# Optimization experiments

Hardware: AMD Instinct MI355X
Metric: run time of the kernel (lower is better)

The kernel has to match this reference:

```python
import jax, jax.numpy as jnp
import numpy as np

N, C, T, V = 16, 128, 128, 25
K, H, OC = 3, 8, 256          # kernel_size subsets, heads, out_channels
HOPMAX = 12                   # hop values in [0, 12); emb_table size HOPMAX
EPS_BN = 1e-5
EPS_NORM = 1e-4


def setup_inputs() -> dict:
    key = jax.random.key(0)
    ks = jax.random.split(key, 12)
    s = 0.05
    x = jax.random.normal(ks[0], (N, C, T, V), jnp.float32)
    hop = jax.random.randint(ks[1], (V, V), 0, HOPMAX)
    emb_table = jax.random.normal(ks[2], (K, H, HOPMAX), jnp.float32) * s
    # A initialized as identity (as in the module) plus small noise for nontrivial grads
    A = jnp.tile(jnp.eye(V, dtype=jnp.float32), (K, H, 1, 1)) \
        + jax.random.normal(ks[3], (K, H, V, V), jnp.float32) * s
    w_block = jax.random.normal(ks[4], (K * OC, C // H), jnp.float32) * s  # grouped 1x1 conv, groups=K*H
    b_block = jax.random.normal(ks[5], (K * OC,), jnp.float32) * s
    bn_gamma = jnp.ones((OC,), jnp.float32)
    bn_beta = jnp.zeros((OC,), jnp.float32)
    res_w = jax.random.normal(ks[6], (OC, C), jnp.float32) * s  # residual 1x1 conv
    res_b = jax.random.normal(ks[7], (OC,), jnp.float32) * s
    res_bn_gamma = jnp.ones((OC,), jnp.float32)
    res_bn_beta = jnp.zeros((OC,), jnp.float32)
    return {"x": x, "hop": hop, "emb_table": emb_table, "A": A,
            "w_block": w_block, "b_block": b_block,
            "bn_gamma": bn_gamma, "bn_beta": bn_beta,
            "res_w": res_w, "res_b": res_b,
            "res_bn_gamma": res_bn_gamma, "res_bn_beta": res_bn_beta}


def _batchnorm(x, gamma, beta):
    # training-mode BatchNorm2d: batch stats over (N, T, V), biased variance
    m = jnp.mean(x, axis=(0, 2, 3), keepdims=True)
    v = jnp.var(x, axis=(0, 2, 3), keepdims=True)
    xn = (x - m) * jax.lax.rsqrt(v + EPS_BN)
    return gamma[None, :, None, None] * xn + beta[None, :, None, None]


def _l2_col_norm(w):
    # torch.norm(w, p=2, dim=-2, keepdim=True) + 1e-4  (in-degree normalization)
    return jnp.sqrt(jnp.sum(w * w, axis=-2, keepdims=True)) + EPS_NORM


def reference(x, hop, emb_table, A, w_block, b_block, bn_gamma, bn_beta,
              res_w, res_b, res_bn_gamma, res_bn_beta):
    n, c, t, v = x.shape
    # residual: 1x1 TemporalConv2d + BN (in_channels != out_channels)
    res = jnp.einsum('nctv,oc->notv', x, res_w) + res_b[None, :, None, None]
    res = _batchnorm(res, res_bn_gamma, res_bn_beta)

    # hop-embedding gather -> [K, H, V, V]; fuse normalized B and A
    B = emb_table[:, :, hop]
    BnA = B / _l2_col_norm(B) + A / _l2_col_norm(A)

    # graph conv: einsum over joint dim v (broadcast over k)
    xh = x.reshape(n, H, c // H, t, v)                      # [N,H,C/H,T,V]
    y = jnp.einsum('nhctv,khvw->nkhctw', xh, BnA)           # [N,K,H,C/H,T,V]
    y = y.reshape(n, K * H, c // H, t, v)                   # groups = K*H

    # grouped 1x1 conv: per-group [C/H -> OC/H] GEMM
    wg = w_block.reshape(K * H, OC // H, c // H)
    out = jnp.einsum('ngctv,goc->ngotv', y, wg)             # [N,K*H,OC/H,T,V]
    out = out.reshape(n, K * OC, t, v) + b_block[None, :, None, None]

    # sum over the K kernel subsets
    out = out.reshape(n, K, OC, t, v).sum(axis=1)
    out = _batchnorm(out, bn_gamma, bn_beta)
    return jax.nn.relu(out + res)
```

## Files before the change

kernel.cpp:

```cpp
#include <hip/hip_runtime.h>
#include <stdint.h>

typedef __attribute__((ext_vector_type(8))) short short8;
typedef __attribute__((ext_vector_type(4))) float f32x4;

#define B_BNA    0ull
#define B_STATS  60416ull
#define B_RESW2  64512ull
#define B_E2     1178624ull
#define B_XB     7994368ull
#define B_MAIN   21625856ull
#define B_RES    47840256ull

#define NTV 51200.0f

__device__ __forceinline__ unsigned short f2bf(float f) {
    unsigned u = __float_as_uint(f);
    return (unsigned short)((u + 0x7fffu + ((u >> 16) & 1u)) >> 16);
}
__device__ __forceinline__ float bf2f(unsigned s) { return __uint_as_float(s << 16); }

__device__ __forceinline__ float wave_sum(float v) {
#pragma unroll
    for (int m = 1; m < 64; m <<= 1) v += __shfl_xor(v, m, 64);
    return v;
}

__device__ __forceinline__ void gl_lds16(const unsigned short* g, unsigned short* l) {
    __builtin_amdgcn_global_load_lds(
        (const __attribute__((address_space(1))) unsigned int*)g,
        (__attribute__((address_space(3))) unsigned int*)l, 16, 0, 0);
}
__device__ __forceinline__ void stage_pair(const unsigned short* g0, const unsigned short* g1,
                                           unsigned short* d) {
    gl_lds16(g0, d);
    gl_lds16(g1, d + 512);
}

__device__ __forceinline__ int swz_idx(int row, int quad) {
    int rowX = row ^ ((row >> 2) & 1);
    return rowX * 32 + ((quad ^ (row & 3)) << 3);
}

__global__ __launch_bounds__(256) void k_prep(const int* __restrict__ hop,
                                              const float* __restrict__ emb,
                                              const float* __restrict__ A,
                                              const float* __restrict__ res_w,
                                              float* __restrict__ bna,
                                              float* __restrict__ stats,
                                              unsigned short* __restrict__ resw2) {
    int g = blockIdx.x, tid = threadIdx.x;
    if (g < 24) {
        if (tid < 25) {
            int w = tid;
            float nb = 0.f, na = 0.f;
            for (int v = 0; v < 25; v++) {
                float e = emb[g*12 + hop[v*25 + w]];
                nb += e*e;
                float a = A[((size_t)g*25 + v)*25 + w];
                na += a*a;
            }
            nb = sqrtf(nb) + 1e-4f;
            na = sqrtf(na) + 1e-4f;
            for (int v = 0; v < 25; v++) {
                float e = emb[g*12 + hop[v*25 + w]];
                float a = A[((size_t)g*25 + v)*25 + w];
                bna[g*625 + v*25 + w] = e/nb + a/na;
            }
        }
    } else if (g == 24) {
#pragma unroll
        for (int i = 0; i < 4; i++) stats[i*256 + tid] = 0.f;
    } else {
        int base = (g - 25) * 4096 + tid * 16;
#pragma unroll
        for (int j = 0; j < 16; j++) resw2[base + j] = f2bf(res_w[base + j]);
    }
}

__global__ __launch_bounds__(256) void k_prep2x(const float* __restrict__ w_block,
                                                const float* __restrict__ bna,
                                                unsigned short* __restrict__ E2,
                                                const float* __restrict__ x,
                                                unsigned short* __restrict__ xb) {
    int bid = blockIdx.x, tid = threadIdx.x;
    if (bid < 128) {
        __shared__ float bl[3*625];
        __shared__ float wl[3*64];
        int half = bid & 1, og = (bid >> 1) & 7, h = bid >> 4;

        for (int i = tid; i < 1875; i += 256) {
            int k3 = i / 625, j = i - k3*625;
            bl[i] = bna[(k3*8 + h)*625 + j];
        }
        if (tid < 192) {
            int k3 = tid >> 6, o = (tid >> 4) & 3, c = tid & 15;
            wl[tid] = w_block[(k3*256 + h*32 + og*4 + o)*16 + c];
        }
        __syncthreads();

        unsigned short* dst = E2 + (size_t)(h*8 + og)*53248;
        int e0 = half * 26624;
        for (int e = e0 + tid; e < e0 + 26624; e += 256) {
            int kc = e >> 12;
            int n  = (e >> 5) & 127;
            int kk = e & 31;
            int k  = kc*32 + kk;
            int o  = n >> 5, w = n & 31;
            float val = 0.f;
            if (k < 400 && w < 25) {
                int c = k / 25, v = k - c*25;
                val = wl[0*64 + o*16 + c] * bl[0*625 + v*25 + w]
                    + wl[1*64 + o*16 + c] * bl[1*625 + v*25 + w]
                    + wl[2*64 + o*16 + c] * bl[2*625 + v*25 + w];
            }
            dst[e] = f2bf(val);
        }
    } else {
        int b = bid - 128;
        int n_ = b >> 7, t_ = b & 127;
        unsigned short* row = xb + (size_t)b * 3328;
        for (int idx = tid; idx < 3200; idx += 256) {
            int c = idx / 25, v = idx - c*25;
            float val = x[(((size_t)n_*128 + c)*128 + t_)*25 + v];
            row[(c >> 4)*416 + (c & 15)*25 + v] = f2bf(val);
        }
        if (tid < 128) row[(tid >> 4)*416 + 400 + (tid & 15)] = 0;
    }
}

__global__ __launch_bounds__(256) void k_mm(const unsigned short* __restrict__ xb,
                                            const unsigned short* __restrict__ E2,
                                            unsigned short* __restrict__ mainp,
                                            const float* __restrict__ x,
                                            const unsigned short* __restrict__ resw2,
                                            unsigned short* __restrict__ resp,
                                            float* __restrict__ stats) {
    __shared__ unsigned short lds[24576];
    int bid = blockIdx.x, tid = threadIdx.x;
    int lane = tid & 63, wave = tid >> 6;
    int wm = wave >> 1, wn = wave & 1;
    int lane15 = lane & 15, quad = lane >> 4;

    int Lrow0 = wave*32 + (lane >> 2), Lq = lane & 3;
    int r0 = Lrow0 ^ ((Lrow0 >> 2) & 1), q0 = Lq ^ (r0 & 3);
    int Lrow1 = Lrow0 + 16;
    int r1 = Lrow1 ^ ((Lrow1 >> 2) & 1), q1 = Lq ^ (r1 & 3);

    const int adoff = wave*1024 + lane*8;

    if (bid < 1024) {
        int h = bid & 7, og = (bid >> 3) & 7, mt = bid >> 6;

        const unsigned short* agA0 = xb + (size_t)(mt*128 + r0)*3328 + h*416 + q0*8;
        const unsigned short* agA1 = xb + (size_t)(mt*128 + r1)*3328 + h*416 + q1*8;
        const unsigned short* eb   = E2 + (size_t)(h*8 + og)*53248;
        const unsigned short* bgB0 = eb + r0*32 + q0*8;
        const unsigned short* bgB1 = eb + r1*32 + q1*8;

        f32x4 acc[4][4] = {};

#pragma unroll
        for (int p = 0; p < 3; p++) {
            int bo = p*8192;
            stage_pair(agA0 + p*32,           agA1 + p*32,           lds + bo + adoff);
            stage_pair(bgB0 + (size_t)p*4096, bgB1 + (size_t)p*4096, lds + bo + 4096 + adoff);
        }

        int bufo = 0;
        for (int kc = 0; kc < 13; kc++) {
            if (kc <= 10)      asm volatile("s_waitcnt vmcnt(8)" ::: "memory");
            else if (kc == 11) asm volatile("s_waitcnt vmcnt(4)" ::: "memory");
            else               asm volatile("s_waitcnt vmcnt(0)" ::: "memory");
            __builtin_amdgcn_s_barrier();

            const unsigned short* Ac = lds + bufo;
            const unsigned short* Bc = lds + bufo + 4096;
            short8 af[4], bq[4];
#pragma unroll
            for (int i = 0; i < 4; i++) {
                af[i] = *(const short8*)&Ac[swz_idx(wm*64 + i*16 + lane15, quad)];
                bq[i] = *(const short8*)&Bc[swz_idx(wn*64 + i*16 + lane15, quad)];
            }
            asm volatile("s_waitcnt lgkmcnt(0)" ::: "memory");
            __builtin_amdgcn_sched_barrier(0);
            __builtin_amdgcn_s_barrier();

            if (kc <= 9) {
                stage_pair(agA0 + (kc+3)*32,            agA1 + (kc+3)*32,
                           lds + bufo + adoff);
                stage_pair(bgB0 + (size_t)(kc+3)*4096,  bgB1 + (size_t)(kc+3)*4096,
                           lds + bufo + 4096 + adoff);
            }
#pragma unroll
            for (int i = 0; i < 4; i++)
#pragma unroll
                for (int j = 0; j < 4; j++)
                    acc[i][j] = __builtin_amdgcn_mfma_f32_16x16x32_bf16(af[i], bq[j], acc[i][j], 0, 0, 0);

            bufo += 8192;
            if (bufo == 24576) bufo = 0;
        }

        float s1[2] = {0.f, 0.f}, s2[2] = {0.f, 0.f};
#pragma unroll
        for (int j = 0; j < 4; j++) {
            int w = (j & 1)*16 + lane15;
            int p = j >> 1;
            if (w < 25) {
                int oc = h*32 + og*4 + wn*2 + p;
#pragma unroll
                for (int i = 0; i < 4; i++) {
                    int tb = wm*64 + i*16 + quad*4;
#pragma unroll
                    for (int r = 0; r < 4; r++) {
                        float val = acc[i][j][r];
                        mainp[((size_t)(mt*256 + oc)*128 + tb + r)*25 + w] = f2bf(val);
                        s1[p] += val;
                        s2[p] = fmaf(val, val, s2[p]);
                    }
                }
            }
        }
#pragma unroll
        for (int p = 0; p < 2; p++) {
            float a = wave_sum(s1[p]);
            float b = wave_sum(s2[p]);
            if (lane == 0) {
                int oc = h*32 + og*4 + wn*2 + p;
                atomicAdd(&stats[oc], a);
                atomicAdd(&stats[256 + oc], b);
            }
        }
    } else {
        int b2 = bid - 1024;
        int nt = (b2 >= 400) ? 1 : 0;
        int mt = b2 - nt*400;

        int n  = mt / 25;
        int off = (mt - n*25) * 128;
        const float* xb2 = x + (size_t)n*409600 + off;

        int c2 = tid >> 4, seg = tid & 15;

        const unsigned short* rb0 = resw2 + (size_t)(nt*128 + r0)*128 + q0*8;
        const unsigned short* rb1 = resw2 + (size_t)(nt*128 + r1)*128 + q1*8;

        f32x4 acc[4][4] = {};

        for (int kc = 0; kc < 4; kc++) {
            stage_pair(rb0 + kc*32, rb1 + kc*32, lds + 4096 + adoff);
            const float* xc0 = xb2 + (size_t)(kc*32 + 2*c2)*3200;
            const float* xc1 = xc0 + 3200;
            int wbase = 2*(c2 & 3), qn = c2 >> 2;
#pragma unroll
            for (int j = 0; j < 8; j++) {
                int m = seg + 16*j;
                unsigned pk = (unsigned)f2bf(xc0[m]) | ((unsigned)f2bf(xc1[m]) << 16);
                *(unsigned*)&lds[swz_idx(m, qn) + wbase] = pk;
            }
            __syncthreads();

            short8 af[4], bq[4];
#pragma unroll
            for (int i = 0; i < 4; i++) {
                af[i] = *(const short8*)&lds[swz_idx(wm*64 + i*16 + lane15, quad)];
                bq[i] = *(const short8*)&lds[4096 + swz_idx(wn*64 + i*16 + lane15, quad)];
            }
#pragma unroll
            for (int i = 0; i < 4; i++)
#pragma unroll
                for (int j = 0; j < 4; j++)
                    acc[i][j] = __builtin_amdgcn_mfma_f32_16x16x32_bf16(af[i], bq[j], acc[i][j], 0, 0, 0);
            __syncthreads();
        }

#pragma unroll
        for (int j = 0; j < 4; j++) {
            int oc = nt*128 + wn*64 + j*16 + lane15;
            float s1 = 0.f, s2 = 0.f;
#pragma unroll
            for (int i = 0; i < 4; i++) {
                int m2b = mt*128 + wm*64 + i*16 + quad*4;
#pragma unroll
                for (int r = 0; r < 4; r++) {
                    float val = acc[i][j][r];
                    int m2e = m2b + r;
                    int b = m2e / 25, v = m2e - b*25;
                    int nn = b >> 7, t = b & 127;
                    resp[((size_t)(nn*256 + oc)*128 + t)*25 + v] = f2bf(val);
                    s1 += val;
                    s2 = fmaf(val, val, s2);
                }
            }
            s1 += __shfl_xor(s1, 16, 64); s1 += __shfl_xor(s1, 32, 64);
            s2 += __shfl_xor(s2, 16, 64); s2 += __shfl_xor(s2, 32, 64);
            if (quad == 0) {
                atomicAdd(&stats[512 + oc], s1);
                atomicAdd(&stats[768 + oc], s2);
            }
        }
    }
}

__global__ __launch_bounds__(256) void k_final(const float* __restrict__ bn_g,
                                               const float* __restrict__ bn_b,
                                               const float* __restrict__ rbn_g,
                                               const float* __restrict__ rbn_b,
                                               const float* __restrict__ stats,
                                               const unsigned short* __restrict__ mainp,
                                               const unsigned short* __restrict__ resp,
                                               float* __restrict__ out) {
    __shared__ float4 cf[8];
    int bid = blockIdx.x, tid = threadIdx.x;
    int base_row = (bid * 1024) / 400;
    if (tid < 8) {
        int row = base_row + tid;
        if (row < 4096) {
            int oc = row & 255;
            const float inv = 1.f / NTV;
            float s1 = stats[oc],       s2 = stats[256 + oc];
            float r1v = stats[512 + oc], r2v = stats[768 + oc];
            float mm = s1*inv, vm = s2*inv - mm*mm;
            float mr = r1v*inv, vr = r2v*inv - mr*mr;
            float a1 = bn_g[oc]  * rsqrtf(vm + 1e-5f);
            float c1 = bn_b[oc]  - a1*mm;
            float a2 = rbn_g[oc] * rsqrtf(vr + 1e-5f);
            float c2 = rbn_b[oc] - a2*mr;
            cf[tid] = make_float4(a1, c1, a2, c2);
        }
    }
    __syncthreads();

    const uint4* m4 = (const uint4*)mainp;
    const uint4* r4 = (const uint4*)resp;
    float4* o4 = (float4*)out;
#pragma unroll
    for (int r = 0; r < 4; r++) {
        int chunk = bid*1024 + r*256 + tid;
        uint4 mu = m4[chunk];
        uint4 ru = r4[chunk];
        float4 C = cf[chunk/400 - base_row];
        float4 f0, f1;
        f0.x = fmaxf(fmaf(C.x, __uint_as_float(mu.x << 16),        C.y)
                   + fmaf(C.z, __uint_as_float(ru.x << 16),        C.w), 0.f);
        f0.y = fmaxf(fmaf(C.x, __uint_as_float(mu.x & 0xffff0000u), C.y)
                   + fmaf(C.z, __uint_as_float(ru.x & 0xffff0000u), C.w), 0.f);
        f0.z = fmaxf(fmaf(C.x, __uint_as_float(mu.y << 16),        C.y)
                   + fmaf(C.z, __uint_as_float(ru.y << 16),        C.w), 0.f);
        f0.w = fmaxf(fmaf(C.x, __uint_as_float(mu.y & 0xffff0000u), C.y)
                   + fmaf(C.z, __uint_as_float(ru.y & 0xffff0000u), C.w), 0.f);
        f1.x = fmaxf(fmaf(C.x, __uint_as_float(mu.z << 16),        C.y)
                   + fmaf(C.z, __uint_as_float(ru.z << 16),        C.w), 0.f);
        f1.y = fmaxf(fmaf(C.x, __uint_as_float(mu.z & 0xffff0000u), C.y)
                   + fmaf(C.z, __uint_as_float(ru.z & 0xffff0000u), C.w), 0.f);
        f1.z = fmaxf(fmaf(C.x, __uint_as_float(mu.w << 16),        C.y)
                   + fmaf(C.z, __uint_as_float(ru.w << 16),        C.w), 0.f);
        f1.w = fmaxf(fmaf(C.x, __uint_as_float(mu.w & 0xffff0000u), C.y)
                   + fmaf(C.z, __uint_as_float(ru.w & 0xffff0000u), C.w), 0.f);
        o4[chunk*2]     = f0;
        o4[chunk*2 + 1] = f1;
    }
}

extern "C" void kernel_launch(void* const* d_in, const int* in_sizes, int n_in,
                              void* d_out, int out_size, void* d_ws, size_t ws_size,
                              hipStream_t stream) {
    const float* x        = (const float*)d_in[0];
    const int*   hop      = (const int*)  d_in[1];
    const float* emb      = (const float*)d_in[2];
    const float* A        = (const float*)d_in[3];
    const float* w_block  = (const float*)d_in[4];
    const float* bn_g     = (const float*)d_in[6];
    const float* bn_b     = (const float*)d_in[7];
    const float* res_w    = (const float*)d_in[8];
    const float* rbn_g    = (const float*)d_in[10];
    const float* rbn_b    = (const float*)d_in[11];
    float* out = (float*)d_out;

    char* ws = (char*)d_ws;
    float*          bna    = (float*)(ws + B_BNA);
    float*          stats  = (float*)(ws + B_STATS);
    unsigned short* resw2  = (unsigned short*)(ws + B_RESW2);
    unsigned short* E2     = (unsigned short*)(ws + B_E2);
    unsigned short* xb     = (unsigned short*)(ws + B_XB);
    unsigned short* mainp  = (unsigned short*)(ws + B_MAIN);
    unsigned short* resp   = (unsigned short*)(ws + B_RES);

    k_prep   <<<33,   256, 0, stream>>>(hop, emb, A, res_w, bna, stats, resw2);
    k_prep2x <<<2176, 256, 0, stream>>>(w_block, bna, E2, x, xb);
    k_mm     <<<1824, 256, 0, stream>>>(xb, E2, mainp, x, resw2, resp, stats);
    k_final  <<<1600, 256, 0, stream>>>(bn_g, bn_b, rbn_g, rbn_b, stats, mainp, resp, out);
}
```

Before: 206.3 us.

## Load MFMA operands directly from global into registers, dropping LDS staging

The main GEMM path no longer stages A and B tiles through a triple-buffered shared-memory ring with barriers. Each wave now loads its own fragments straight from global memory into registers, double-buffered in software, which removes the LDS round trip and the block barriers and shrinks LDS to just what the residual path needs, allowing more resident blocks. In exchange, waves sharing a tile each fetch the same data from global or L2, giving up the reuse LDS provided. Per-lane 16-byte loads strided by 3328 elements may also coalesce poorly, and load latency is hidden by only one step of prefetch.

```diff
diff --git a/kernel.cpp b/kernel.cpp
--- a/kernel.cpp
+++ b/kernel.cpp
@@ -136,70 +136,56 @@
                                             const unsigned short* __restrict__ resw2,
                                             unsigned short* __restrict__ resp,
                                             float* __restrict__ stats) {
-    __shared__ unsigned short lds[24576];
+    __shared__ unsigned short lds[8192];
     int bid = blockIdx.x, tid = threadIdx.x;
     int lane = tid & 63, wave = tid >> 6;
     int wm = wave >> 1, wn = wave & 1;
     int lane15 = lane & 15, quad = lane >> 4;
 
-    int Lrow0 = wave*32 + (lane >> 2), Lq = lane & 3;
-    int r0 = Lrow0 ^ ((Lrow0 >> 2) & 1), q0 = Lq ^ (r0 & 3);
-    int Lrow1 = Lrow0 + 16;
-    int r1 = Lrow1 ^ ((Lrow1 >> 2) & 1), q1 = Lq ^ (r1 & 3);
-
-    const int adoff = wave*1024 + lane*8;
-
     if (bid < 1024) {
         int h = bid & 7, og = (bid >> 3) & 7, mt = bid >> 6;
 
-        const unsigned short* agA0 = xb + (size_t)(mt*128 + r0)*3328 + h*416 + q0*8;
-        const unsigned short* agA1 = xb + (size_t)(mt*128 + r1)*3328 + h*416 + q1*8;
-        const unsigned short* eb   = E2 + (size_t)(h*8 + og)*53248;
-        const unsigned short* bgB0 = eb + r0*32 + q0*8;
-        const unsigned short* bgB1 = eb + r1*32 + q1*8;
+        const unsigned short* Abase = xb + (size_t)(mt*128 + wm*64 + lane15)*3328
+                                         + h*416 + quad*8;
+        const unsigned short* Bbase = E2 + (size_t)(h*8 + og)*53248
+                                         + (wn*64 + lane15)*32 + quad*8;
+
+        auto loadA = [&](short8* d, int kc) {
+#pragma unroll
+            for (int i = 0; i < 4; i++)
+                d[i] = *(const short8*)(Abase + (size_t)i*16*3328 + kc*32);
+        };
+        auto loadB = [&](short8* d, int kc) {
+#pragma unroll
+            for (int j = 0; j < 4; j++)
+                d[j] = *(const short8*)(Bbase + j*512 + (size_t)kc*4096);
+        };
 
         f32x4 acc[4][4] = {};
-
-#pragma unroll
-        for (int p = 0; p < 3; p++) {
-            int bo = p*8192;
-            stage_pair(agA0 + p*32,           agA1 + p*32,           lds + bo + adoff);
-            stage_pair(bgB0 + (size_t)p*4096, bgB1 + (size_t)p*4096, lds + bo + 4096 + adoff);
-        }
-
-        int bufo = 0;
-        for (int kc = 0; kc < 13; kc++) {
-            if (kc <= 10)      asm volatile("s_waitcnt vmcnt(8)" ::: "memory");
-            else if (kc == 11) asm volatile("s_waitcnt vmcnt(4)" ::: "memory");
-            else               asm volatile("s_waitcnt vmcnt(0)" ::: "memory");
-            __builtin_amdgcn_s_barrier();
-
-            const unsigned short* Ac = lds + bufo;
-            const unsigned short* Bc = lds + bufo + 4096;
-            short8 af[4], bq[4];
-#pragma unroll
-            for (int i = 0; i < 4; i++) {
-                af[i] = *(const short8*)&Ac[swz_idx(wm*64 + i*16 + lane15, quad)];
-                bq[i] = *(const short8*)&Bc[swz_idx(wn*64 + i*16 + lane15, quad)];
-            }
-            asm volatile("s_waitcnt lgkmcnt(0)" ::: "memory");
-            __builtin_amdgcn_sched_barrier(0);
-            __builtin_amdgcn_s_barrier();
-
-            if (kc <= 9) {
-                stage_pair(agA0 + (kc+3)*32,            agA1 + (kc+3)*32,
-                           lds + bufo + adoff);
-                stage_pair(bgB0 + (size_t)(kc+3)*4096,  bgB1 + (size_t)(kc+3)*4096,
-                           lds + bufo + 4096 + adoff);
+        short8 aA[4], bA[4], aB[4], bB[4];
+
+        loadA(aA, 0); loadB(bA, 0);
+        for (int kc = 0; kc < 13; kc += 2) {
+            if (kc + 1 < 13) {
+                loadA(aB, kc + 1); loadB(bB, kc + 1);
+                __builtin_amdgcn_sched_barrier(0);
             }
 #pragma unroll
             for (int i = 0; i < 4; i++)
 #pragma unroll
                 for (int j = 0; j < 4; j++)
-                    acc[i][j] = __builtin_amdgcn_mfma_f32_16x16x32_bf16(af[i], bq[j], acc[i][j], 0, 0, 0);
-
-            bufo += 8192;
-            if (bufo == 24576) bufo = 0;
+                    acc[i][j] = __builtin_amdgcn_mfma_f32_16x16x32_bf16(aA[i], bA[j], acc[i][j], 0, 0, 0);
+            if (kc + 1 < 13) {
+                if (kc + 2 < 13) {
+                    loadA(aA, kc + 2); loadB(bA, kc + 2);
+                    __builtin_amdgcn_sched_barrier(0);
+                }
+#pragma unroll
+                for (int i = 0; i < 4; i++)
+#pragma unroll
+                    for (int j = 0; j < 4; j++)
+                        acc[i][j] = __builtin_amdgcn_mfma_f32_16x16x32_bf16(aB[i], bB[j], acc[i][j], 0, 0, 0);
+            }
         }
 
         float s1[2] = {0.f, 0.f}, s2[2] = {0.f, 0.f};
@@ -236,6 +222,12 @@
         int b2 = bid - 1024;
         int nt = (b2 >= 400) ? 1 : 0;
         int mt = b2 - nt*400;
+
+        int Lrow0 = wave*32 + (lane >> 2), Lq = lane & 3;
+        int r0 = Lrow0 ^ ((Lrow0 >> 2) & 1), q0 = Lq ^ (r0 & 3);
+        int Lrow1 = Lrow0 + 16;
+        int r1 = Lrow1 ^ ((Lrow1 >> 2) & 1), q1 = Lq ^ (r1 & 3);
+        const int adoff = wave*1024 + lane*8;
 
         int n  = mt / 25;
         int off = (mt - n*25) * 128;
```

Result: slower. 247.7 us (+20.0%).

## Fuse prep kernels and switch GEMM staging to double buffering

Applied to the files above, without the earlier changes.

Merges the BnA/stats/res-weight prep kernel into the E2/xb prep kernel, so each E2 block recomputes its head's normalized adjacency directly into shared memory. This removes one launch and a global intermediate buffer. The main GEMM kernel moves from a triple- to a double-buffered LDS pipeline, reducing LDS use to allow higher occupancy at the cost of a shallower prefetch depth.

```diff
diff --git a/kernel.cpp b/kernel.cpp
--- a/kernel.cpp
+++ b/kernel.cpp
@@ -4,7 +4,6 @@
 typedef __attribute__((ext_vector_type(8))) short short8;
 typedef __attribute__((ext_vector_type(4))) float f32x4;
 
-#define B_BNA    0ull
 #define B_STATS  60416ull
 #define B_RESW2  64512ull
 #define B_E2     1178624ull
@@ -42,17 +41,25 @@
     return rowX * 32 + ((quad ^ (row & 3)) << 3);
 }
 
-__global__ __launch_bounds__(256) void k_prep(const int* __restrict__ hop,
-                                              const float* __restrict__ emb,
-                                              const float* __restrict__ A,
-                                              const float* __restrict__ res_w,
-                                              float* __restrict__ bna,
-                                              float* __restrict__ stats,
-                                              unsigned short* __restrict__ resw2) {
-    int g = blockIdx.x, tid = threadIdx.x;
-    if (g < 24) {
-        if (tid < 25) {
-            int w = tid;
+__global__ __launch_bounds__(256) void k_prep2x(const int* __restrict__ hop,
+                                                const float* __restrict__ emb,
+                                                const float* __restrict__ A,
+                                                const float* __restrict__ res_w,
+                                                const float* __restrict__ w_block,
+                                                unsigned short* __restrict__ E2,
+                                                const float* __restrict__ x,
+                                                unsigned short* __restrict__ xb,
+                                                float* __restrict__ stats,
+                                                unsigned short* __restrict__ resw2) {
+    int bid = blockIdx.x, tid = threadIdx.x;
+    if (bid < 128) {
+        __shared__ float bl[3*625];
+        __shared__ float wl[3*64];
+        int half = bid & 1, og = (bid >> 1) & 7, h = bid >> 4;
+
+        if (tid < 75) {
+            int k3 = tid / 25, w = tid - k3*25;
+            int g = k3*8 + h;
             float nb = 0.f, na = 0.f;
             for (int v = 0; v < 25; v++) {
                 float e = emb[g*12 + hop[v*25 + w]];
@@ -65,33 +72,8 @@
             for (int v = 0; v < 25; v++) {
                 float e = emb[g*12 + hop[v*25 + w]];
                 float a = A[((size_t)g*25 + v)*25 + w];
-                bna[g*625 + v*25 + w] = e/nb + a/na;
-            }
-        }
-    } else if (g == 24) {
-#pragma unroll
-        for (int i = 0; i < 4; i++) stats[i*256 + tid] = 0.f;
-    } else {
-        int base = (g - 25) * 4096 + tid * 16;
-#pragma unroll
-        for (int j = 0; j < 16; j++) resw2[base + j] = f2bf(res_w[base + j]);
-    }
-}
-
-__global__ __launch_bounds__(256) void k_prep2x(const float* __restrict__ w_block,
-                                                const float* __restrict__ bna,
-                                                unsigned short* __restrict__ E2,
-                                                const float* __restrict__ x,
-                                                unsigned short* __restrict__ xb) {
-    int bid = blockIdx.x, tid = threadIdx.x;
-    if (bid < 128) {
-        __shared__ float bl[3*625];
-        __shared__ float wl[3*64];
-        int half = bid & 1, og = (bid >> 1) & 7, h = bid >> 4;
-
-        for (int i = tid; i < 1875; i += 256) {
-            int k3 = i / 625, j = i - k3*625;
-            bl[i] = bna[(k3*8 + h)*625 + j];
+                bl[k3*625 + v*25 + w] = e/nb + a/na;
+            }
         }
         if (tid < 192) {
             int k3 = tid >> 6, o = (tid >> 4) & 3, c = tid & 15;
@@ -116,7 +98,7 @@
             }
             dst[e] = f2bf(val);
         }
-    } else {
+    } else if (bid < 2176) {
         int b = bid - 128;
         int n_ = b >> 7, t_ = b & 127;
         unsigned short* row = xb + (size_t)b * 3328;
@@ -126,6 +108,13 @@
             row[(c >> 4)*416 + (c & 15)*25 + v] = f2bf(val);
         }
         if (tid < 128) row[(tid >> 4)*416 + 400 + (tid & 15)] = 0;
+    } else if (bid == 2176) {
+#pragma unroll
+        for (int i = 0; i < 4; i++) stats[i*256 + tid] = 0.f;
+    } else {
+        int base = (bid - 2177) * 4096 + tid * 16;
+#pragma unroll
+        for (int j = 0; j < 16; j++) resw2[base + j] = f2bf(res_w[base + j]);
     }
 }
 
@@ -136,7 +125,7 @@
                                             const unsigned short* __restrict__ resw2,
                                             unsigned short* __restrict__ resp,
                                             float* __restrict__ stats) {
-    __shared__ unsigned short lds[24576];
+    __shared__ unsigned short lds[16384];
     int bid = blockIdx.x, tid = threadIdx.x;
     int lane = tid & 63, wave = tid >> 6;
     int wm = wave >> 1, wn = wave & 1;
@@ -146,7 +135,6 @@
     int r0 = Lrow0 ^ ((Lrow0 >> 2) & 1), q0 = Lq ^ (r0 & 3);
     int Lrow1 = Lrow0 + 16;
     int r1 = Lrow1 ^ ((Lrow1 >> 2) & 1), q1 = Lq ^ (r1 & 3);
-
     const int adoff = wave*1024 + lane*8;
 
     if (bid < 1024) {
@@ -160,22 +148,19 @@
 
         f32x4 acc[4][4] = {};
 
-#pragma unroll
-        for (int p = 0; p < 3; p++) {
-            int bo = p*8192;
-            stage_pair(agA0 + p*32,           agA1 + p*32,           lds + bo + adoff);
-            stage_pair(bgB0 + (size_t)p*4096, bgB1 + (size_t)p*4096, lds + bo + 4096 + adoff);
-        }
-
-        int bufo = 0;
+        stage_pair(agA0,        agA1,        lds + adoff);
+        stage_pair(bgB0,        bgB1,        lds + 4096 + adoff);
+        stage_pair(agA0 + 32,   agA1 + 32,   lds + 8192 + adoff);
+        stage_pair(bgB0 + 4096, bgB1 + 4096, lds + 8192 + 4096 + adoff);
+
         for (int kc = 0; kc < 13; kc++) {
-            if (kc <= 10)      asm volatile("s_waitcnt vmcnt(8)" ::: "memory");
-            else if (kc == 11) asm volatile("s_waitcnt vmcnt(4)" ::: "memory");
-            else               asm volatile("s_waitcnt vmcnt(0)" ::: "memory");
+            if (kc < 12) asm volatile("s_waitcnt vmcnt(4)" ::: "memory");
+            else         asm volatile("s_waitcnt vmcnt(0)" ::: "memory");
             __builtin_amdgcn_s_barrier();
 
-            const unsigned short* Ac = lds + bufo;
-            const unsigned short* Bc = lds + bufo + 4096;
+            int cur = (kc & 1) << 13;
+            const unsigned short* Ac = lds + cur;
+            const unsigned short* Bc = lds + cur + 4096;
             short8 af[4], bq[4];
 #pragma unroll
             for (int i = 0; i < 4; i++) {
@@ -186,20 +171,18 @@
             __builtin_amdgcn_sched_barrier(0);
             __builtin_amdgcn_s_barrier();
 
-            if (kc <= 9) {
-                stage_pair(agA0 + (kc+3)*32,            agA1 + (kc+3)*32,
-                           lds + bufo + adoff);
-                stage_pair(bgB0 + (size_t)(kc+3)*4096,  bgB1 + (size_t)(kc+3)*4096,
-                           lds + bufo + 4096 + adoff);
+            if (kc < 11) {
+                stage_pair(agA0 + (kc+2)*32,           agA1 + (kc+2)*32,
+                           lds + cur + adoff);
+                stage_pair(bgB0 + (size_t)(kc+2)*4096, bgB1 + (size_t)(kc+2)*4096,
+                           lds + cur + 4096 + adoff);
+                __builtin_amdgcn_sched_barrier(0);
             }
 #pragma unroll
             for (int i = 0; i < 4; i++)
 #pragma unroll
                 for (int j = 0; j < 4; j++)
                     acc[i][j] = __builtin_amdgcn_mfma_f32_16x16x32_bf16(af[i], bq[j], acc[i][j], 0, 0, 0);
-
-            bufo += 8192;
-            if (bufo == 24576) bufo = 0;
         }
 
         float s1[2] = {0.f, 0.f}, s2[2] = {0.f, 0.f};
@@ -379,7 +362,6 @@
     float* out = (float*)d_out;
 
     char* ws = (char*)d_ws;
-    float*          bna    = (float*)(ws + B_BNA);
     float*          stats  = (float*)(ws + B_STATS);
     unsigned short* resw2  = (unsigned short*)(ws + B_RESW2);
     unsigned short* E2     = (unsigned short*)(ws + B_E2);
@@ -387,8 +369,7 @@
     unsigned short* mainp  = (unsigned short*)(ws + B_MAIN);
     unsigned short* resp   = (unsigned short*)(ws + B_RES);
 
-    k_prep   <<<33,   256, 0, stream>>>(hop, emb, A, res_w, bna, stats, resw2);
-    k_prep2x <<<2176, 256, 0, stream>>>(w_block, bna, E2, x, xb);
+    k_prep2x <<<2185, 256, 0, stream>>>(hop, emb, A, res_w, w_block, E2, x, xb, stats, resw2);
     k_mm     <<<1824, 256, 0, stream>>>(xb, E2, mainp, x, resw2, resp, stats);
     k_final  <<<1600, 256, 0, stream>>>(bn_g, bn_b, rbn_g, rbn_b, stats, mainp, resp, out);
 }
```

New measurement: 216.5 us. +4.9%, slower.
